# Kernel tuning notes

Hardware: AMD Instinct MI355X
Metric: run time of the kernel (lower is better)

## Reference

```python
import jax, jax.numpy as jnp
import numpy as np

STALK_DIM = 16
N_NODES = 50000
N_EDGES = 400000
HIDDEN = 64


def setup_inputs() -> dict:
    key = jax.random.key(0)
    k1, k2, k3, k4 = jax.random.split(key, 4)
    d = STALK_DIM
    x = jax.random.normal(k1, (N_NODES, d), dtype=jnp.float32)
    edge_index = jax.random.randint(k2, (2, N_EDGES), 0, N_NODES, dtype=jnp.int64)
    W1 = jax.random.normal(k3, (HIDDEN, 2 * d), dtype=jnp.float32) * (1.0 / np.sqrt(2 * d))
    b1 = jnp.zeros((HIDDEN,), dtype=jnp.float32)
    W2 = jax.random.normal(k4, (d, HIDDEN), dtype=jnp.float32) * (1.0 / np.sqrt(HIDDEN))
    b2 = jnp.zeros((d,), dtype=jnp.float32)
    return {"x": x, "edge_index": edge_index, "W1": W1, "b1": b1, "W2": W2, "b2": b2}


def reference(x, edge_index, W1, b1, W2, b2):
    d = x.shape[1]
    n = x.shape[0]
    src, dst = edge_index[0], edge_index[1]
    xs, xd = x[src], x[dst]  # [E, d]

    def reflection(a, b):
        h = jax.nn.relu(jnp.concatenate([a, b], axis=1) @ W1.T + b1)
        return h @ W2.T + b2  # [E, d]

    def householder(v):
        # F.normalize(v, dim=1): v / max(||v||, 1e-12)
        vn = v / jnp.maximum(jnp.linalg.norm(v, axis=1, keepdims=True), 1e-12)
        return jnp.eye(d, dtype=v.dtype)[None] - 2.0 * vn[:, :, None] * vn[:, None, :]

    F_s = householder(reflection(xs, xd))  # [E, d, d]
    F_d = householder(reflection(xd, xs))  # [E, d, d]
    L_sd = -jnp.einsum('eki,ekj->eij', F_s, F_d)  # -F_s^T @ F_d, [E, d, d]

    # degrees: both endpoints of every edge contribute 1
    ones_e = jnp.ones(src.shape[0], dtype=x.dtype)
    deg = jnp.zeros(n, dtype=x.dtype).at[src].add(ones_e).at[dst].add(ones_e)
    deg_inv_sqrt = 1.0 / jnp.sqrt(jnp.maximum(deg, 1e-5))
    # D_inv_sqrt is scalar*I per node, so normalization is a scalar coefficient per edge
    coef = deg_inv_sqrt[src] * deg_inv_sqrt[dst]  # [E]

    # out[s] -= D^-1/2_s L D^-1/2_d x[d] ; out[d] -= D^-1/2_d L^T D^-1/2_s x[s]
    msg_s = coef[:, None] * jnp.einsum('eij,ej->ei', L_sd, xd)  # goes to src
    msg_d = coef[:, None] * jnp.einsum('eji,ej->ei', L_sd, xs)  # goes to dst

    out = x - jnp.zeros_like(x).at[src].add(msg_s) - jnp.zeros_like(x).at[dst].add(msg_d)
    return jax.nn.relu(out)
```

## Files before the change

### kernel.cpp

```cpp
#include <hip/hip_runtime.h>
#include <hip/hip_bf16.h>
#include <hip/hip_fp16.h>

#define N_NODES 50000
#define N_EDGES 400000
#define D 16
#define HID 64

#define SCAN_B 256
#define SCAN_G ((N_NODES + SCAN_B - 1) / SCAN_B)

typedef unsigned short ushort_t;

#define CNT4_OFF  0
#define DEG_OFF   (4 * N_NODES)
#define OFF_OFF   (5 * N_NODES)
#define CUR_OFF   (6 * N_NODES + 1)
#define BS_OFF    (7 * N_NODES + 1)
#define MSG_OFF_I (((BS_OFF + SCAN_G) + 3) & ~3)
#define PREP_OFF  (MSG_OFF_I + 2 * N_EDGES * D)
#define PREP_DW   (64 * 64 + 16)
#define CSR_NEEDED_BYTES ((size_t)(PREP_OFF + PREP_DW) * 4 + 64)

#define FB_NDEG   (N_NODES)
#define FB_NACC   (N_NODES * D)
#define FB_FLAGS  (FB_NDEG + FB_NACC)

__device__ __forceinline__ float bf_bits(ushort_t us) {
    return __uint_as_float(((unsigned)us) << 16);
}
__device__ __forceinline__ float lo_bf(unsigned u) { return __uint_as_float(u << 16); }
__device__ __forceinline__ float hi_bf(unsigned u) { return __uint_as_float(u & 0xffff0000u); }
__device__ __forceinline__ ushort_t f2bf(float v) {
    unsigned u = __float_as_uint(v);
    unsigned r = (u + 0x7fffu + ((u >> 16) & 1u)) >> 16;
    return (ushort_t)r;
}
__device__ __forceinline__ float ld_f(const void* p, int idx, int f32) {
    return f32 ? ((const float*)p)[idx]
               : bf_bits(((const ushort_t*)p)[idx]);
}

__device__ __forceinline__ void load16(const void* __restrict__ p, long long base,
                                       int f32, float* o) {
    if (f32) {
        const float4* q = (const float4*)((const float*)p + base);
        float4 a = q[0], b = q[1], c = q[2], d = q[3];
        o[0]=a.x; o[1]=a.y; o[2]=a.z; o[3]=a.w;
        o[4]=b.x; o[5]=b.y; o[6]=b.z; o[7]=b.w;
        o[8]=c.x; o[9]=c.y; o[10]=c.z; o[11]=c.w;
        o[12]=d.x; o[13]=d.y; o[14]=d.z; o[15]=d.w;
    } else {
        const uint4* q = (const uint4*)((const ushort_t*)p + base);
        uint4 a = q[0], b = q[1];
        unsigned u[8] = {a.x, a.y, a.z, a.w, b.x, b.y, b.z, b.w};
#pragma unroll
        for (int k = 0; k < 8; k++) {
            o[2 * k]     = lo_bf(u[k]);
            o[2 * k + 1] = hi_bf(u[k]);
        }
    }
}

__device__ __forceinline__ void load_edge(const void* __restrict__ ei, int e, int is64,
                                          int& s, int& d) {
    if (is64) {
        const long long* p = (const long long*)ei;
        s = (int)p[e];
        d = (int)p[N_EDGES + e];
    } else {
        const int* p = (const int*)ei;
        s = p[e];
        d = p[N_EDGES + e];
    }
}

__device__ __forceinline__ void detect_flags_par(const void* x, const void* ei,
                                                 int* flags) {
    int t = threadIdx.x;
    if (t < 64) {
        const ushort_t* h = (const ushort_t*)x;
        int bad = 0;
#pragma unroll
        for (int k = 0; k < 4; k++) {
            float v = bf_bits(h[4 * t + k]);
            if (!(v == v) || fabsf(v) > 1.0e6f) bad = 1;
        }
        unsigned long long mb = __ballot(bad);
        const long long* p = (const long long*)ei;
        int bad64 = 0;
        if (t < 16) {
            long long v = p[t];
            bad64 = (v < 0 || v >= N_NODES) ? 1 : 0;
        }
        unsigned long long m64 = __ballot(bad64);
        if (t == 0) {
            flags[0] = mb ? 1 : 0;
            flags[1] = m64 ? 0 : 1;
        }
    }
}

__device__ __forceinline__ void stage_weights(
    const void* W1, const void* b1, const void* W2, const void* b2, int f32,
    float* sW1, float* sW2t, float* sb1, float* sb2)
{
    int t = threadIdx.x;
    for (int idx = t; idx < HID * 2 * D; idx += blockDim.x)
        sW1[idx] = ld_f(W1, idx, f32);
    for (int idx = t; idx < HID * D; idx += blockDim.x) {
        int j = idx / D, i = idx % D;
        sW2t[idx] = ld_f(W2, i * HID + j, f32);
    }
    if (t < HID) sb1[t] = ld_f(b1, t, f32);
    if (t < D)  sb2[t] = ld_f(b2, t, f32);
}

__device__ __forceinline__ void edge_math_v4(
    const float* __restrict__ sW1, const float* __restrict__ sW2t,
    const float* __restrict__ sb1, const float* __restrict__ sb2,
    const float* xs, const float* xd, float coef,
    float* ms, float* md)
{
    float vs[D], vd[D];
#pragma unroll
    for (int i = 0; i < D; i++) { vs[i] = sb2[i]; vd[i] = sb2[i]; }
#pragma unroll 4
    for (int j = 0; j < HID; j++) {
        float hs = sb1[j], hd = sb1[j];
        const float4* w4 = (const float4*)&sW1[j * 2 * D];
#pragma unroll
        for (int t = 0; t < 4; t++) {
            float4 wv = w4[t];
            int k = 4 * t;
            hs = fmaf(wv.x, xs[k],     hs); hd = fmaf(wv.x, xd[k],     hd);
            hs = fmaf(wv.y, xs[k + 1], hs); hd = fmaf(wv.y, xd[k + 1], hd);
            hs = fmaf(wv.z, xs[k + 2], hs); hd = fmaf(wv.z, xd[k + 2], hd);
            hs = fmaf(wv.w, xs[k + 3], hs); hd = fmaf(wv.w, xd[k + 3], hd);
        }
#pragma unroll
        for (int t = 0; t < 4; t++) {
            float4 wv = w4[4 + t];
            int k = 4 * t;
            hs = fmaf(wv.x, xd[k],     hs); hd = fmaf(wv.x, xs[k],     hd);
            hs = fmaf(wv.y, xd[k + 1], hs); hd = fmaf(wv.y, xs[k + 1], hd);
            hs = fmaf(wv.z, xd[k + 2], hs); hd = fmaf(wv.z, xs[k + 2], hd);
            hs = fmaf(wv.w, xd[k + 3], hs); hd = fmaf(wv.w, xs[k + 3], hd);
        }
        hs = fmaxf(hs, 0.0f);
        hd = fmaxf(hd, 0.0f);
        const float4* w24 = (const float4*)&sW2t[j * D];
#pragma unroll
        for (int t = 0; t < 4; t++) {
            float4 u = w24[t];
            int i = 4 * t;
            vs[i]     = fmaf(u.x, hs, vs[i]);     vd[i]     = fmaf(u.x, hd, vd[i]);
            vs[i + 1] = fmaf(u.y, hs, vs[i + 1]); vd[i + 1] = fmaf(u.y, hd, vd[i + 1]);
            vs[i + 2] = fmaf(u.z, hs, vs[i + 2]); vd[i + 2] = fmaf(u.z, hd, vd[i + 2]);
            vs[i + 3] = fmaf(u.w, hs, vs[i + 3]); vd[i + 3] = fmaf(u.w, hd, vd[i + 3]);
        }
    }
    float ns = 0.0f, nd = 0.0f;
#pragma unroll
    for (int i = 0; i < D; i++) { ns = fmaf(vs[i], vs[i], ns); nd = fmaf(vd[i], vd[i], nd); }
    float is_ = 1.0f / fmaxf(sqrtf(ns), 1e-12f);
    float id_ = 1.0f / fmaxf(sqrtf(nd), 1e-12f);
#pragma unroll
    for (int i = 0; i < D; i++) { vs[i] *= is_; vd[i] *= id_; }
    float dot1 = 0.0f;
#pragma unroll
    for (int i = 0; i < D; i++) dot1 = fmaf(vd[i], xd[i], dot1);
#pragma unroll
    for (int i = 0; i < D; i++) ms[i] = fmaf(-2.0f * dot1, vd[i], xd[i]);
    float dot2 = 0.0f;
#pragma unroll
    for (int i = 0; i < D; i++) dot2 = fmaf(vs[i], ms[i], dot2);
#pragma unroll
    for (int i = 0; i < D; i++) ms[i] = coef * fmaf(-2.0f * dot2, vs[i], ms[i]);
    float dot3 = 0.0f;
#pragma unroll
    for (int i = 0; i < D; i++) dot3 = fmaf(vs[i], xs[i], dot3);
#pragma unroll
    for (int i = 0; i < D; i++) md[i] = fmaf(-2.0f * dot3, vs[i], xs[i]);
    float dot4 = 0.0f;
#pragma unroll
    for (int i = 0; i < D; i++) dot4 = fmaf(vd[i], md[i], dot4);
#pragma unroll
    for (int i = 0; i < D; i++) md[i] = coef * fmaf(-2.0f * dot4, vd[i], md[i]);
}

__global__ void csr_count_kernel(const void* __restrict__ ei,
                                 const void* __restrict__ x,
                                 const void* __restrict__ W1,
                                 const void* __restrict__ b1,
                                 const void* __restrict__ W2,
                                 const void* __restrict__ b2,
                                 int* __restrict__ wsI) {
    __shared__ int sfl[2];
    detect_flags_par(x, ei, sfl);
    __syncthreads();
    int i64 = sfl[1];

    if (blockIdx.x == 0) {
        float* pf = (float*)(wsI + PREP_OFF);
        const ushort_t* W1b = (const ushort_t*)W1;
        const ushort_t* W2b = (const ushort_t*)W2;
        const ushort_t* b1b = (const ushort_t*)b1;
        const ushort_t* b2b = (const ushort_t*)b2;
        for (int idx = threadIdx.x; idx < 64 * 64; idx += 256) {
            int j = idx >> 6, w = idx & 63;
            float val = 0.0f;
            if (w < 32)      val = bf_bits(W1b[j * 32 + w]);
            else if (w < 48) val = bf_bits(W2b[(w - 32) * HID + j]);
            else if (w == 48) val = bf_bits(b1b[j]);
            pf[idx] = val;
        }
        if (threadIdx.x < D)
            pf[64 * 64 + threadIdx.x] = bf_bits(b2b[threadIdx.x]);
    }

    int e = blockIdx.x * blockDim.x + threadIdx.x;
    if (e >= N_EDGES) return;
    int s, d;
    load_edge(ei, e, i64, s, d);
    int r = (e & 3) * N_NODES;
    atomicAdd(&wsI[CNT4_OFF + r + s], 1);
    atomicAdd(&wsI[CNT4_OFF + r + d], 1);
}

__global__ __launch_bounds__(SCAN_B) void csr_scan1_kernel(int* __restrict__ wsI) {
    __shared__ int sm[SCAN_B];
    int t = threadIdx.x;
    int g = blockIdx.x * SCAN_B + t;
    int c = 0;
    if (g < N_NODES) {
        c = wsI[CNT4_OFF + g] + wsI[CNT4_OFF + N_NODES + g]
          + wsI[CNT4_OFF + 2 * N_NODES + g] + wsI[CNT4_OFF + 3 * N_NODES + g];
        wsI[DEG_OFF + g] = c;
    }
    sm[t] = c;
    __syncthreads();
    for (int st = SCAN_B / 2; st > 0; st >>= 1) {
        if (t < st) sm[t] += sm[t + st];
        __syncthreads();
    }
    if (t == 0) wsI[BS_OFF + blockIdx.x] = sm[0];
}

__global__ __launch_bounds__(SCAN_B) void csr_scan3_kernel(int* __restrict__ wsI) {
    __shared__ int sB[SCAN_B];
    __shared__ int sm[SCAN_B];
    int t = threadIdx.x;
    int bsv = (t < SCAN_G) ? wsI[BS_OFF + t] : 0;
    sB[t] = bsv;
    __syncthreads();
    for (int st = 1; st < SCAN_B; st <<= 1) {
        int u = (t >= st) ? sB[t - st] : 0;
        __syncthreads();
        sB[t] += u;
        __syncthreads();
    }
    int blockBase = sB[blockIdx.x] - wsI[BS_OFF + blockIdx.x];

    int g = blockIdx.x * SCAN_B + t;
    int c = (g < N_NODES) ? wsI[DEG_OFF + g] : 0;
    sm[t] = c;
    __syncthreads();
    for (int st = 1; st < SCAN_B; st <<= 1) {
        int u = (t >= st) ? sm[t - st] : 0;
        __syncthreads();
        sm[t] += u;
        __syncthreads();
    }
    int excl = sm[t] - c + blockBase;
    if (g < N_NODES) {
        wsI[OFF_OFF + g] = excl;
        wsI[CUR_OFF + g] = excl;
        if (g == N_NODES - 1) wsI[OFF_OFF + N_NODES] = excl + c;
    }
}

__global__ __launch_bounds__(256) void csr_edge_kernel(
    const void* __restrict__ x,
    const void* __restrict__ ei,
    const void* __restrict__ W1,
    const void* __restrict__ b1,
    const void* __restrict__ W2,
    const void* __restrict__ b2,
    const float* __restrict__ prep,
    int* __restrict__ wsI)
{
    __shared__ __align__(16) float sW1f[HID * 2 * D];
    __shared__ __align__(16) float sW2tf[HID * D];
    __shared__ float sb1[HID];
    __shared__ float sb2[D];
    __shared__ int sfl[2];

    detect_flags_par(x, ei, sfl);
    __syncthreads();
    int f32 = sfl[0], i64 = sfl[1];
    int t = threadIdx.x;

    if (f32) {
        for (int idx = t; idx < HID * 2 * D; idx += 256)
            sW1f[idx] = ld_f(W1, idx, 1);
        for (int idx = t; idx < HID * D; idx += 256) {
            int j = idx / D, i = idx % D;
            sW2tf[idx] = ld_f(W2, i * HID + j, 1);
        }
        if (t < HID) sb1[t] = ld_f(b1, t, 1);
        if (t < D)  sb2[t] = ld_f(b2, t, 1);
        __syncthreads();
    }

    int e = blockIdx.x * 256 + t;
    if (e >= N_EDGES) return;

    int s, d;
    load_edge(ei, e, i64, s, d);
    float degs = (float)wsI[DEG_OFF + s];
    float degd = (float)wsI[DEG_OFF + d];
    float coef = (1.0f / sqrtf(fmaxf(degs, 1e-5f))) * (1.0f / sqrtf(fmaxf(degd, 1e-5f)));
    float* msg = (float*)(wsI + MSG_OFF_I);

    float xs[D], xd[D];
    load16(x, (long long)s * D, f32, xs);
    load16(x, (long long)d * D, f32, xd);

    float ms[D], md[D];
    if (!f32) {
        const float* b2f = prep + 64 * 64;
        float vs[D], vd[D];
#pragma unroll
        for (int i = 0; i < D; i++) { vs[i] = b2f[i]; vd[i] = b2f[i]; }

#pragma unroll 1
        for (int j = 0; j < HID; j++) {
            const float* w = prep + (j << 6);
            float b1j = w[48];
            float hs0 = b1j, hs1 = 0.0f, hd0 = b1j, hd1 = 0.0f;
#pragma unroll
            for (int k = 0; k < 8; k++) {
                hs0 = fmaf(w[k],     xs[k],     hs0);
                hd0 = fmaf(w[k],     xd[k],     hd0);
                hs1 = fmaf(w[8 + k], xs[8 + k], hs1);
                hd1 = fmaf(w[8 + k], xd[8 + k], hd1);
            }
#pragma unroll
            for (int k = 0; k < 8; k++) {
                hs0 = fmaf(w[16 + k], xd[k],     hs0);
                hd0 = fmaf(w[16 + k], xs[k],     hd0);
                hs1 = fmaf(w[24 + k], xd[8 + k], hs1);
                hd1 = fmaf(w[24 + k], xs[8 + k], hd1);
            }
            float hs = fmaxf(hs0 + hs1, 0.0f);
            float hd = fmaxf(hd0 + hd1, 0.0f);
#pragma unroll
            for (int i = 0; i < D; i++) {
                vs[i] = fmaf(w[32 + i], hs, vs[i]);
                vd[i] = fmaf(w[32 + i], hd, vd[i]);
            }
        }

        float ns = 0.0f, nd = 0.0f;
#pragma unroll
        for (int i = 0; i < D; i++) { ns = fmaf(vs[i], vs[i], ns); nd = fmaf(vd[i], vd[i], nd); }
        float is_ = 1.0f / fmaxf(sqrtf(ns), 1e-12f);
        float id_ = 1.0f / fmaxf(sqrtf(nd), 1e-12f);
#pragma unroll
        for (int i = 0; i < D; i++) { vs[i] *= is_; vd[i] *= id_; }

        float dot1 = 0.0f;
#pragma unroll
        for (int i = 0; i < D; i++) dot1 = fmaf(vd[i], xd[i], dot1);
#pragma unroll
        for (int i = 0; i < D; i++) ms[i] = fmaf(-2.0f * dot1, vd[i], xd[i]);
        float dot2 = 0.0f;
#pragma unroll
        for (int i = 0; i < D; i++) dot2 = fmaf(vs[i], ms[i], dot2);
#pragma unroll
        for (int i = 0; i < D; i++) ms[i] = coef * fmaf(-2.0f * dot2, vs[i], ms[i]);
        float dot3 = 0.0f;
#pragma unroll
        for (int i = 0; i < D; i++) dot3 = fmaf(vs[i], xs[i], dot3);
#pragma unroll
        for (int i = 0; i < D; i++) md[i] = fmaf(-2.0f * dot3, vs[i], xs[i]);
        float dot4 = 0.0f;
#pragma unroll
        for (int i = 0; i < D; i++) dot4 = fmaf(vd[i], md[i], dot4);
#pragma unroll
        for (int i = 0; i < D; i++) md[i] = coef * fmaf(-2.0f * dot4, vd[i], md[i]);
    } else {
        edge_math_v4(sW1f, sW2tf, sb1, sb2, xs, xd, coef, ms, md);
    }

    int slot_s = atomicAdd(&wsI[CUR_OFF + s], 1);
    float4* m0 = (float4*)(msg + (long long)slot_s * D);
    m0[0] = make_float4(ms[0], ms[1], ms[2], ms[3]);
    m0[1] = make_float4(ms[4], ms[5], ms[6], ms[7]);
    m0[2] = make_float4(ms[8], ms[9], ms[10], ms[11]);
    m0[3] = make_float4(ms[12], ms[13], ms[14], ms[15]);
    int slot_d = atomicAdd(&wsI[CUR_OFF + d], 1);
    float4* m1 = (float4*)(msg + (long long)slot_d * D);
    m1[0] = make_float4(md[0], md[1], md[2], md[3]);
    m1[1] = make_float4(md[4], md[5], md[6], md[7]);
    m1[2] = make_float4(md[8], md[9], md[10], md[11]);
    m1[3] = make_float4(md[12], md[13], md[14], md[15]);
}

__global__ __launch_bounds__(256) void csr_gather_kernel(
    const void* __restrict__ x,
    const void* __restrict__ ei,
    const int* __restrict__ wsI,
    void* __restrict__ out)
{
    __shared__ int sfl[2];
    detect_flags_par(x, ei, sfl);
    __syncthreads();
    int f32 = sfl[0];

    int n = blockIdx.x * 64 + (threadIdx.x >> 2);
    int c = threadIdx.x & 3;
    if (n >= N_NODES) return;

    const int* off = wsI + OFF_OFF;
    const float4* msg4 = (const float4*)(wsI + MSG_OFF_I);

    int beg = off[n], end = off[n + 1];
    float4 a = make_float4(0.0f, 0.0f, 0.0f, 0.0f);
    int it = beg;
    for (; it + 2 <= end; it += 2) {
        float4 u = msg4[(long long)it * 4 + c];
        float4 v = msg4[(long long)(it + 1) * 4 + c];
        a.x += u.x + v.x; a.y += u.y + v.y; a.z += u.z + v.z; a.w += u.w + v.w;
    }
    if (it < end) {
        float4 u = msg4[(long long)it * 4 + c];
        a.x += u.x; a.y += u.y; a.z += u.z; a.w += u.w;
    }

    long long xb = (long long)n * D + 4 * c;
    float4 xv;
    if (f32) {
        xv = *(const float4*)((const float*)x + xb);
    } else {
        uint2 u = *(const uint2*)((const ushort_t*)x + xb);
        xv.x = lo_bf(u.x); xv.y = hi_bf(u.x);
        xv.z = lo_bf(u.y); xv.w = hi_bf(u.y);
    }
    float4 r;
    r.x = fmaxf(xv.x + a.x, 0.0f);
    r.y = fmaxf(xv.y + a.y, 0.0f);
    r.z = fmaxf(xv.z + a.z, 0.0f);
    r.w = fmaxf(xv.w + a.w, 0.0f);
    if (f32) {
        *(float4*)((float*)out + xb) = r;
    } else {
        uint2 o;
        o.x = (unsigned)f2bf(r.x) | ((unsigned)f2bf(r.y) << 16);
        o.y = (unsigned)f2bf(r.z) | ((unsigned)f2bf(r.w) << 16);
        *(uint2*)((ushort_t*)out + xb) = o;
    }
}

__global__ void fb_init_kernel(float* __restrict__ ws,
                               const void* __restrict__ x,
                               const void* __restrict__ ei) {
    int i = blockIdx.x * blockDim.x + threadIdx.x;
    if (i < FB_FLAGS) ws[i] = 0.0f;
    if (blockIdx.x == 0)
        detect_flags_par(x, ei, (int*)(ws + FB_FLAGS));
}

__global__ void fb_deg_kernel(const void* __restrict__ ei, float* __restrict__ ws) {
    int i64 = ((const int*)(ws + FB_FLAGS))[1];
    int e = blockIdx.x * blockDim.x + threadIdx.x;
    if (e >= N_EDGES) return;
    int s, d;
    load_edge(ei, e, i64, s, d);
    atomicAdd(&ws[s], 1.0f);
    atomicAdd(&ws[d], 1.0f);
}

__global__ __launch_bounds__(256) void fb_edge_kernel(
    const void* __restrict__ x, const void* __restrict__ ei,
    const void* __restrict__ W1, const void* __restrict__ b1,
    const void* __restrict__ W2, const void* __restrict__ b2,
    float* __restrict__ ws)
{
    __shared__ __align__(16) float sW1[HID * 2 * D];
    __shared__ __align__(16) float sW2t[HID * D];
    __shared__ float sb1[HID];
    __shared__ float sb2[D];
    const int* flags = (const int*)(ws + FB_FLAGS);
    int f32 = flags[0], i64 = flags[1];
    stage_weights(W1, b1, W2, b2, f32, sW1, sW2t, sb1, sb2);
    __syncthreads();
    int e = blockIdx.x * blockDim.x + threadIdx.x;
    if (e >= N_EDGES) return;
    int s, d;
    load_edge(ei, e, i64, s, d);
    float xs[D], xd[D];
    load16(x, (long long)s * D, f32, xs);
    load16(x, (long long)d * D, f32, xd);
    float coef = (1.0f / sqrtf(fmaxf(ws[s], 1e-5f))) * (1.0f / sqrtf(fmaxf(ws[d], 1e-5f)));
    float ms[D], md[D];
    edge_math_v4(sW1, sW2t, sb1, sb2, xs, xd, coef, ms, md);
    float* acc = ws + FB_NDEG;
#pragma unroll
    for (int i = 0; i < D; i++) atomicAdd(&acc[(long long)s * D + i], ms[i]);
#pragma unroll
    for (int i = 0; i < D; i++) atomicAdd(&acc[(long long)d * D + i], md[i]);
}

__global__ void fb_finalize_kernel(const void* __restrict__ x,
                                   const float* __restrict__ ws,
                                   void* __restrict__ out)
{
    int f32 = ((const int*)(ws + FB_FLAGS))[0];
    const float* acc = ws + FB_NDEG;
    int i = blockIdx.x * blockDim.x + threadIdx.x;
    if (i >= FB_NACC) return;
    float v = ld_f(x, i, f32) + acc[i];
    v = fmaxf(v, 0.0f);
    if (f32) ((float*)out)[i] = v;
    else     ((__hip_bfloat16*)out)[i] = __float2bfloat16(v);
}

extern "C" void kernel_launch(void* const* d_in, const int* in_sizes, int n_in,
                              void* d_out, int out_size, void* d_ws, size_t ws_size,
                              hipStream_t stream)
{
    const void* x  = d_in[0];
    const void* ei = d_in[1];
    const void* W1 = d_in[2];
    const void* b1 = d_in[3];
    const void* W2 = d_in[4];
    const void* b2 = d_in[5];

    int blk = 256;
    if (ws_size >= CSR_NEEDED_BYTES) {
        int* wsI = (int*)d_ws;
        hipMemsetAsync(d_ws, 0, (size_t)4 * N_NODES * sizeof(int), stream);
        csr_count_kernel<<<(N_EDGES + blk - 1) / blk, blk, 0, stream>>>(ei, x, W1, b1, W2, b2, wsI);
        csr_scan1_kernel<<<SCAN_G, SCAN_B, 0, stream>>>(wsI);
        csr_scan3_kernel<<<SCAN_G, SCAN_B, 0, stream>>>(wsI);
        csr_edge_kernel<<<(N_EDGES + blk - 1) / blk, blk, 0, stream>>>(
            x, ei, W1, b1, W2, b2, (const float*)(wsI + PREP_OFF), wsI);
        csr_gather_kernel<<<(N_NODES + 63) / 64, blk, 0, stream>>>(x, ei, wsI, d_out);
    } else {
        float* ws = (float*)d_ws;
        fb_init_kernel<<<(FB_FLAGS + blk - 1) / blk, blk, 0, stream>>>(ws, x, ei);
        fb_deg_kernel<<<(N_EDGES + blk - 1) / blk, blk, 0, stream>>>(ei, ws);
        fb_edge_kernel<<<(N_EDGES + blk - 1) / blk, blk, 0, stream>>>(x, ei, W1, b1, W2, b2, ws);
        fb_finalize_kernel<<<(FB_NACC + blk - 1) / blk, blk, 0, stream>>>(x, ws, d_out);
    }
}
```

Before: 204.7 us.

## Precompute per-node first-layer projections to avoid per-edge W1 matmul

Splits the first MLP layer W1·[a;b] into per-node halves A=W1a·x+b1 and B=W1b·x, computed once per node inside the scan kernel and stored in a new workspace region. The edge kernel then forms hidden units as relu(A[s]+B[d]) and relu(A[d]+B[s]), removing the 64x32 per-edge dot products and leaving only the second layer. In exchange each edge reads two 512-byte node rows, the workspace needs N*128 extra floats, and the path runs only for bf16 inputs when the workspace is large enough.

Result: no change. 205.8 us (+0.6%).

```diff
diff --git a/kernel.cpp b/kernel.cpp
--- a/kernel.cpp
+++ b/kernel.cpp
@@ -17,10 +17,13 @@
 #define OFF_OFF   (5 * N_NODES)
 #define CUR_OFF   (6 * N_NODES + 1)
 #define BS_OFF    (7 * N_NODES + 1)
-#define MSG_OFF_I (((BS_OFF + SCAN_G) + 3) & ~3)
+#define MSG_OFF_I (((BS_OFF + SCAN_G) + 15) & ~15)
 #define PREP_OFF  (MSG_OFF_I + 2 * N_EDGES * D)
-#define PREP_DW   (64 * 64 + 16)
-#define CSR_NEEDED_BYTES ((size_t)(PREP_OFF + PREP_DW) * 4 + 64)
+#define PREP_DW   (64 * 64 + 16 + 64 * 16)
+#define AB_OFF    (PREP_OFF + PREP_DW)
+#define AB_DW     (N_NODES * 2 * HID)
+#define CSR_NEEDED_BYTES ((size_t)(AB_OFF) * 4 + 64)
+#define NEW_NEEDED_BYTES ((size_t)(AB_OFF + AB_DW) * 4 + 64)
 
 #define FB_NDEG   (N_NODES)
 #define FB_NACC   (N_NODES * D)
@@ -189,211 +192,77 @@
     for (int i = 0; i < D; i++) md[i] = coef * fmaf(-2.0f * dot4, vd[i], md[i]);
 }
 
-__global__ void csr_count_kernel(const void* __restrict__ ei,
-                                 const void* __restrict__ x,
-                                 const void* __restrict__ W1,
-                                 const void* __restrict__ b1,
-                                 const void* __restrict__ W2,
-                                 const void* __restrict__ b2,
-                                 int* __restrict__ wsI) {
-    __shared__ int sfl[2];
-    detect_flags_par(x, ei, sfl);
-    __syncthreads();
-    int i64 = sfl[1];
-
-    if (blockIdx.x == 0) {
-        float* pf = (float*)(wsI + PREP_OFF);
-        const ushort_t* W1b = (const ushort_t*)W1;
-        const ushort_t* W2b = (const ushort_t*)W2;
-        const ushort_t* b1b = (const ushort_t*)b1;
-        const ushort_t* b2b = (const ushort_t*)b2;
-        for (int idx = threadIdx.x; idx < 64 * 64; idx += 256) {
-            int j = idx >> 6, w = idx & 63;
-            float val = 0.0f;
-            if (w < 32)      val = bf_bits(W1b[j * 32 + w]);
-            else if (w < 48) val = bf_bits(W2b[(w - 32) * HID + j]);
-            else if (w == 48) val = bf_bits(b1b[j]);
-            pf[idx] = val;
-        }
-        if (threadIdx.x < D)
-            pf[64 * 64 + threadIdx.x] = bf_bits(b2b[threadIdx.x]);
-    }
-
-    int e = blockIdx.x * blockDim.x + threadIdx.x;
-    if (e >= N_EDGES) return;
-    int s, d;
-    load_edge(ei, e, i64, s, d);
-    int r = (e & 3) * N_NODES;
-    atomicAdd(&wsI[CNT4_OFF + r + s], 1);
-    atomicAdd(&wsI[CNT4_OFF + r + d], 1);
-}
-
-__global__ __launch_bounds__(SCAN_B) void csr_scan1_kernel(int* __restrict__ wsI) {
-    __shared__ int sm[SCAN_B];
-    int t = threadIdx.x;
-    int g = blockIdx.x * SCAN_B + t;
-    int c = 0;
-    if (g < N_NODES) {
-        c = wsI[CNT4_OFF + g] + wsI[CNT4_OFF + N_NODES + g]
-          + wsI[CNT4_OFF + 2 * N_NODES + g] + wsI[CNT4_OFF + 3 * N_NODES + g];
-        wsI[DEG_OFF + g] = c;
-    }
-    sm[t] = c;
-    __syncthreads();
-    for (int st = SCAN_B / 2; st > 0; st >>= 1) {
-        if (t < st) sm[t] += sm[t + st];
-        __syncthreads();
-    }
-    if (t == 0) wsI[BS_OFF + blockIdx.x] = sm[0];
-}
-
-__global__ __launch_bounds__(SCAN_B) void csr_scan3_kernel(int* __restrict__ wsI) {
-    __shared__ int sB[SCAN_B];
-    __shared__ int sm[SCAN_B];
-    int t = threadIdx.x;
-    int bsv = (t < SCAN_G) ? wsI[BS_OFF + t] : 0;
-    sB[t] = bsv;
-    __syncthreads();
-    for (int st = 1; st < SCAN_B; st <<= 1) {
-        int u = (t >= st) ? sB[t - st] : 0;
-        __syncthreads();
-        sB[t] += u;
-        __syncthreads();
-    }
-    int blockBase = sB[blockIdx.x] - wsI[BS_OFF + blockIdx.x];
-
-    int g = blockIdx.x * SCAN_B + t;
-    int c = (g < N_NODES) ? wsI[DEG_OFF + g] : 0;
-    sm[t] = c;
-    __syncthreads();
-    for (int st = 1; st < SCAN_B; st <<= 1) {
-        int u = (t >= st) ? sm[t - st] : 0;
-        __syncthreads();
-        sm[t] += u;
-        __syncthreads();
-    }
-    int excl = sm[t] - c + blockBase;
-    if (g < N_NODES) {
-        wsI[OFF_OFF + g] = excl;
-        wsI[CUR_OFF + g] = excl;
-        if (g == N_NODES - 1) wsI[OFF_OFF + N_NODES] = excl + c;
-    }
-}
-
-__global__ __launch_bounds__(256) void csr_edge_kernel(
-    const void* __restrict__ x,
-    const void* __restrict__ ei,
-    const void* __restrict__ W1,
-    const void* __restrict__ b1,
-    const void* __restrict__ W2,
-    const void* __restrict__ b2,
+__device__ __forceinline__ void edge_math_prep(
     const float* __restrict__ prep,
-    int* __restrict__ wsI)
-{
-    __shared__ __align__(16) float sW1f[HID * 2 * D];
-    __shared__ __align__(16) float sW2tf[HID * D];
-    __shared__ float sb1[HID];
-    __shared__ float sb2[D];
-    __shared__ int sfl[2];
-
-    detect_flags_par(x, ei, sfl);
-    __syncthreads();
-    int f32 = sfl[0], i64 = sfl[1];
-    int t = threadIdx.x;
-
-    if (f32) {
-        for (int idx = t; idx < HID * 2 * D; idx += 256)
-            sW1f[idx] = ld_f(W1, idx, 1);
-        for (int idx = t; idx < HID * D; idx += 256) {
-            int j = idx / D, i = idx % D;
-            sW2tf[idx] = ld_f(W2, i * HID + j, 1);
-        }
-        if (t < HID) sb1[t] = ld_f(b1, t, 1);
-        if (t < D)  sb2[t] = ld_f(b2, t, 1);
-        __syncthreads();
-    }
-
-    int e = blockIdx.x * 256 + t;
-    if (e >= N_EDGES) return;
-
-    int s, d;
-    load_edge(ei, e, i64, s, d);
-    float degs = (float)wsI[DEG_OFF + s];
-    float degd = (float)wsI[DEG_OFF + d];
-    float coef = (1.0f / sqrtf(fmaxf(degs, 1e-5f))) * (1.0f / sqrtf(fmaxf(degd, 1e-5f)));
-    float* msg = (float*)(wsI + MSG_OFF_I);
-
-    float xs[D], xd[D];
-    load16(x, (long long)s * D, f32, xs);
-    load16(x, (long long)d * D, f32, xd);
-
-    float ms[D], md[D];
-    if (!f32) {
-        const float* b2f = prep + 64 * 64;
-        float vs[D], vd[D];
-#pragma unroll
-        for (int i = 0; i < D; i++) { vs[i] = b2f[i]; vd[i] = b2f[i]; }
+    const float* xs, const float* xd, float coef,
+    float* ms, float* md)
+{
+    const float* b2f = prep + 64 * 64;
+    float vs[D], vd[D];
+#pragma unroll
+    for (int i = 0; i < D; i++) { vs[i] = b2f[i]; vd[i] = b2f[i]; }
 
 #pragma unroll 1
-        for (int j = 0; j < HID; j++) {
-            const float* w = prep + (j << 6);
-            float b1j = w[48];
-            float hs0 = b1j, hs1 = 0.0f, hd0 = b1j, hd1 = 0.0f;
-#pragma unroll
-            for (int k = 0; k < 8; k++) {
-                hs0 = fmaf(w[k],     xs[k],     hs0);
-                hd0 = fmaf(w[k],     xd[k],     hd0);
-                hs1 = fmaf(w[8 + k], xs[8 + k], hs1);
-                hd1 = fmaf(w[8 + k], xd[8 + k], hd1);
-            }
-#pragma unroll
-            for (int k = 0; k < 8; k++) {
-                hs0 = fmaf(w[16 + k], xd[k],     hs0);
-                hd0 = fmaf(w[16 + k], xs[k],     hd0);
-                hs1 = fmaf(w[24 + k], xd[8 + k], hs1);
-                hd1 = fmaf(w[24 + k], xs[8 + k], hd1);
-            }
-            float hs = fmaxf(hs0 + hs1, 0.0f);
-            float hd = fmaxf(hd0 + hd1, 0.0f);
-#pragma unroll
-            for (int i = 0; i < D; i++) {
-                vs[i] = fmaf(w[32 + i], hs, vs[i]);
-                vd[i] = fmaf(w[32 + i], hd, vd[i]);
-            }
-        }
-
-        float ns = 0.0f, nd = 0.0f;
-#pragma unroll
-        for (int i = 0; i < D; i++) { ns = fmaf(vs[i], vs[i], ns); nd = fmaf(vd[i], vd[i], nd); }
-        float is_ = 1.0f / fmaxf(sqrtf(ns), 1e-12f);
-        float id_ = 1.0f / fmaxf(sqrtf(nd), 1e-12f);
-#pragma unroll
-        for (int i = 0; i < D; i++) { vs[i] *= is_; vd[i] *= id_; }
-
-        float dot1 = 0.0f;
-#pragma unroll
-        for (int i = 0; i < D; i++) dot1 = fmaf(vd[i], xd[i], dot1);
-#pragma unroll
-        for (int i = 0; i < D; i++) ms[i] = fmaf(-2.0f * dot1, vd[i], xd[i]);
-        float dot2 = 0.0f;
-#pragma unroll
-        for (int i = 0; i < D; i++) dot2 = fmaf(vs[i], ms[i], dot2);
-#pragma unroll
-        for (int i = 0; i < D; i++) ms[i] = coef * fmaf(-2.0f * dot2, vs[i], ms[i]);
-        float dot3 = 0.0f;
-#pragma unroll
-        for (int i = 0; i < D; i++) dot3 = fmaf(vs[i], xs[i], dot3);
-#pragma unroll
-        for (int i = 0; i < D; i++) md[i] = fmaf(-2.0f * dot3, vs[i], xs[i]);
-        float dot4 = 0.0f;
-#pragma unroll
-        for (int i = 0; i < D; i++) dot4 = fmaf(vd[i], md[i], dot4);
-#pragma unroll
-        for (int i = 0; i < D; i++) md[i] = coef * fmaf(-2.0f * dot4, vd[i], md[i]);
-    } else {
-        edge_math_v4(sW1f, sW2tf, sb1, sb2, xs, xd, coef, ms, md);
-    }
-
+    for (int j = 0; j < HID; j++) {
+        const float* w = prep + (j << 6);
+        float b1j = w[48];
+        float hs0 = b1j, hs1 = 0.0f, hd0 = b1j, hd1 = 0.0f;
+#pragma unroll
+        for (int k = 0; k < 8; k++) {
+            hs0 = fmaf(w[k],     xs[k],     hs0);
+            hd0 = fmaf(w[k],     xd[k],     hd0);
+            hs1 = fmaf(w[8 + k], xs[8 + k], hs1);
+            hd1 = fmaf(w[8 + k], xd[8 + k], hd1);
+        }
+#pragma unroll
+        for (int k = 0; k < 8; k++) {
+            hs0 = fmaf(w[16 + k], xd[k],     hs0);
+            hd0 = fmaf(w[16 + k], xs[k],     hd0);
+            hs1 = fmaf(w[24 + k], xd[8 + k], hs1);
+            hd1 = fmaf(w[24 + k], xs[8 + k], hd1);
+        }
+        float hs = fmaxf(hs0 + hs1, 0.0f);
+        float hd = fmaxf(hd0 + hd1, 0.0f);
+#pragma unroll
+        for (int i = 0; i < D; i++) {
+            vs[i] = fmaf(w[32 + i], hs, vs[i]);
+            vd[i] = fmaf(w[32 + i], hd, vd[i]);
+        }
+    }
+
+    float ns = 0.0f, nd = 0.0f;
+#pragma unroll
+    for (int i = 0; i < D; i++) { ns = fmaf(vs[i], vs[i], ns); nd = fmaf(vd[i], vd[i], nd); }
+    float is_ = 1.0f / fmaxf(sqrtf(ns), 1e-12f);
+    float id_ = 1.0f / fmaxf(sqrtf(nd), 1e-12f);
+#pragma unroll
+    for (int i = 0; i < D; i++) { vs[i] *= is_; vd[i] *= id_; }
+
+    float dot1 = 0.0f;
+#pragma unroll
+    for (int i = 0; i < D; i++) dot1 = fmaf(vd[i], xd[i], dot1);
+#pragma unroll
+    for (int i = 0; i < D; i++) ms[i] = fmaf(-2.0f * dot1, vd[i], xd[i]);
+    float dot2 = 0.0f;
+#pragma unroll
+    for (int i = 0; i < D; i++) dot2 = fmaf(vs[i], ms[i], dot2);
+#pragma unroll
+    for (int i = 0; i < D; i++) ms[i] = coef * fmaf(-2.0f * dot2, vs[i], ms[i]);
+    float dot3 = 0.0f;
+#pragma unroll
+    for (int i = 0; i < D; i++) dot3 = fmaf(vs[i], xs[i], dot3);
+#pragma unroll
+    for (int i = 0; i < D; i++) md[i] = fmaf(-2.0f * dot3, vs[i], xs[i]);
+    float dot4 = 0.0f;
+#pragma unroll
+    for (int i = 0; i < D; i++) dot4 = fmaf(vd[i], md[i], dot4);
+#pragma unroll
+    for (int i = 0; i < D; i++) md[i] = coef * fmaf(-2.0f * dot4, vd[i], md[i]);
+}
+
+__device__ __forceinline__ void write_msgs(int* __restrict__ wsI, float* __restrict__ msg,
+                                           int s, int d, const float* ms, const float* md)
+{
     int slot_s = atomicAdd(&wsI[CUR_OFF + s], 1);
     float4* m0 = (float4*)(msg + (long long)slot_s * D);
     m0[0] = make_float4(ms[0], ms[1], ms[2], ms[3]);
@@ -408,21 +277,36 @@
     m1[3] = make_float4(md[12], md[13], md[14], md[15]);
 }
 
-__global__ __launch_bounds__(256) void csr_gather_kernel(
-    const void* __restrict__ x,
-    const void* __restrict__ ei,
-    const int* __restrict__ wsI,
-    void* __restrict__ out)
-{
-    __shared__ int sfl[2];
-    detect_flags_par(x, ei, sfl);
-    __syncthreads();
-    int f32 = sfl[0];
-
-    int n = blockIdx.x * 64 + (threadIdx.x >> 2);
-    int c = threadIdx.x & 3;
-    if (n >= N_NODES) return;
-
+__device__ __forceinline__ void pack_prep(const void* W1, const void* b1,
+                                          const void* W2, const void* b2,
+                                          int* __restrict__ wsI)
+{
+    float* pf = (float*)(wsI + PREP_OFF);
+    const ushort_t* W1b = (const ushort_t*)W1;
+    const ushort_t* W2b = (const ushort_t*)W2;
+    const ushort_t* b1b = (const ushort_t*)b1;
+    const ushort_t* b2b = (const ushort_t*)b2;
+    for (int idx = threadIdx.x; idx < 64 * 64; idx += 256) {
+        int j = idx >> 6, w = idx & 63;
+        float val = 0.0f;
+        if (w < 32)      val = bf_bits(W1b[j * 32 + w]);
+        else if (w < 48) val = bf_bits(W2b[(w - 32) * HID + j]);
+        else if (w == 48) val = bf_bits(b1b[j]);
+        pf[idx] = val;
+    }
+    if (threadIdx.x < D)
+        pf[64 * 64 + threadIdx.x] = bf_bits(b2b[threadIdx.x]);
+    for (int idx = threadIdx.x; idx < HID * D; idx += 256) {
+        int j = idx >> 4, i = idx & 15;
+        pf[64 * 64 + 16 + idx] = bf_bits(W2b[i * HID + j]);
+    }
+}
+
+__device__ __forceinline__ void gather_node(int n, int c, int f32,
+                                            const int* __restrict__ wsI,
+                                            const void* __restrict__ x,
+                                            void* __restrict__ out)
+{
     const int* off = wsI + OFF_OFF;
     const float4* msg4 = (const float4*)(wsI + MSG_OFF_I);
 
@@ -463,6 +347,258 @@
     }
 }
 
+__global__ void csr_count_kernel(const void* __restrict__ ei,
+                                 const void* __restrict__ x,
+                                 const void* __restrict__ W1,
+                                 const void* __restrict__ b1,
+                                 const void* __restrict__ W2,
+                                 const void* __restrict__ b2,
+                                 int* __restrict__ wsI) {
+    __shared__ int sfl[2];
+    detect_flags_par(x, ei, sfl);
+    __syncthreads();
+    int i64 = sfl[1];
+
+    if (blockIdx.x == 0) pack_prep(W1, b1, W2, b2, wsI);
+
+    int e = blockIdx.x * blockDim.x + threadIdx.x;
+    if (e >= N_EDGES) return;
+    int s, d;
+    load_edge(ei, e, i64, s, d);
+    int r = (e & 3) * N_NODES;
+    atomicAdd(&wsI[CNT4_OFF + r + s], 1);
+    atomicAdd(&wsI[CNT4_OFF + r + d], 1);
+}
+
+__global__ __launch_bounds__(SCAN_B) void csr_scan1_kernel(
+    int* __restrict__ wsI,
+    const void* __restrict__ x,
+    const void* __restrict__ ei,
+    const void* __restrict__ W1,
+    const void* __restrict__ b1,
+    int useAB)
+{
+    __shared__ int sm[SCAN_B];
+    __shared__ int sfl[2];
+    detect_flags_par(x, ei, sfl);
+    __syncthreads();
+    int f32 = sfl[0];
+
+    int t = threadIdx.x;
+    int g = blockIdx.x * SCAN_B + t;
+    int c = 0;
+    if (g < N_NODES) {
+        c = wsI[CNT4_OFF + g] + wsI[CNT4_OFF + N_NODES + g]
+          + wsI[CNT4_OFF + 2 * N_NODES + g] + wsI[CNT4_OFF + 3 * N_NODES + g];
+        wsI[DEG_OFF + g] = c;
+    }
+    sm[t] = c;
+    __syncthreads();
+    for (int st = SCAN_B / 2; st > 0; st >>= 1) {
+        if (t < st) sm[t] += sm[t + st];
+        __syncthreads();
+    }
+    if (t == 0) wsI[BS_OFF + blockIdx.x] = sm[0];
+
+    if (useAB && !f32 && g < N_NODES) {
+        const ushort_t* b1b = (const ushort_t*)b1;
+        const unsigned* W1w = (const unsigned*)W1;
+        float xr[D];
+        load16(x, (long long)g * D, 0, xr);
+        float* ab = (float*)(wsI + AB_OFF) + (long long)g * 2 * HID;
+#pragma unroll 1
+        for (int j4 = 0; j4 < 16; j4++) {
+            float4 a4, b4;
+#pragma unroll
+            for (int r = 0; r < 4; r++) {
+                int j = 4 * j4 + r;
+                const unsigned* w = W1w + j * 16;
+                float a = bf_bits(b1b[j]);
+                float bb = 0.0f;
+#pragma unroll
+                for (int k = 0; k < 8; k++) {
+                    unsigned wk = w[k];
+                    a = fmaf(lo_bf(wk), xr[2 * k],     a);
+                    a = fmaf(hi_bf(wk), xr[2 * k + 1], a);
+                }
+#pragma unroll
+                for (int k = 0; k < 8; k++) {
+                    unsigned wk = w[8 + k];
+                    bb = fmaf(lo_bf(wk), xr[2 * k],     bb);
+                    bb = fmaf(hi_bf(wk), xr[2 * k + 1], bb);
+                }
+                (&a4.x)[r] = a;
+                (&b4.x)[r] = bb;
+            }
+            *(float4*)(ab + 4 * j4)       = a4;
+            *(float4*)(ab + HID + 4 * j4) = b4;
+        }
+    }
+}
+
+__global__ __launch_bounds__(SCAN_B) void csr_scan3_kernel(int* __restrict__ wsI) {
+    __shared__ int sB[SCAN_B];
+    __shared__ int sm[SCAN_B];
+    int t = threadIdx.x;
+    int bsv = (t < SCAN_G) ? wsI[BS_OFF + t] : 0;
+    sB[t] = bsv;
+    __syncthreads();
+    for (int st = 1; st < SCAN_B; st <<= 1) {
+        int u = (t >= st) ? sB[t - st] : 0;
+        __syncthreads();
+        sB[t] += u;
+        __syncthreads();
+    }
+    int blockBase = sB[blockIdx.x] - wsI[BS_OFF + blockIdx.x];
+
+    int g = blockIdx.x * SCAN_B + t;
+    int c = (g < N_NODES) ? wsI[DEG_OFF + g] : 0;
+    sm[t] = c;
+    __syncthreads();
+    for (int st = 1; st < SCAN_B; st <<= 1) {
+        int u = (t >= st) ? sm[t - st] : 0;
+        __syncthreads();
+        sm[t] += u;
+        __syncthreads();
+    }
+    int excl = sm[t] - c + blockBase;
+    if (g < N_NODES) {
+        wsI[OFF_OFF + g] = excl;
+        wsI[CUR_OFF + g] = excl;
+        if (g == N_NODES - 1) wsI[OFF_OFF + N_NODES] = excl + c;
+    }
+}
+
+__global__ __launch_bounds__(256) void csr_edge_kernel(
+    const void* __restrict__ x,
+    const void* __restrict__ ei,
+    const void* __restrict__ W1,
+    const void* __restrict__ b1,
+    const void* __restrict__ W2,
+    const void* __restrict__ b2,
+    const float* __restrict__ prep,
+    int* __restrict__ wsI,
+    int useAB)
+{
+    __shared__ __align__(16) float sW1f[HID * 2 * D];
+    __shared__ __align__(16) float sW2tf[HID * D];
+    __shared__ float sb1[HID];
+    __shared__ float sb2[D];
+    __shared__ int sfl[2];
+
+    detect_flags_par(x, ei, sfl);
+    __syncthreads();
+    int f32 = sfl[0], i64 = sfl[1];
+    int t = threadIdx.x;
+
+    if (f32) {
+        stage_weights(W1, b1, W2, b2, 1, sW1f, sW2tf, sb1, sb2);
+        __syncthreads();
+    }
+
+    int e = blockIdx.x * 256 + t;
+    if (e >= N_EDGES) return;
+
+    int s, d;
+    load_edge(ei, e, i64, s, d);
+    float degs = (float)wsI[DEG_OFF + s];
+    float degd = (float)wsI[DEG_OFF + d];
+    float coef = (1.0f / sqrtf(fmaxf(degs, 1e-5f))) * (1.0f / sqrtf(fmaxf(degd, 1e-5f)));
+    float* msg = (float*)(wsI + MSG_OFF_I);
+
+    if (!f32 && useAB) {
+        const float* AB = (const float*)(wsI + AB_OFF);
+        const float* ns_ = AB + (long long)s * 2 * HID;
+        const float* nd_ = AB + (long long)d * 2 * HID;
+        const float* b2f = prep + 64 * 64;
+        const float* w2t = prep + 64 * 64 + 16;
+
+        float vs[D], vd[D];
+#pragma unroll
+        for (int i = 0; i < D; i++) { vs[i] = b2f[i]; vd[i] = b2f[i]; }
+
+#pragma unroll 1
+        for (int jj = 0; jj < 16; jj++) {
+            float4 as4 = *(const float4*)(ns_ + 4 * jj);
+            float4 bs4 = *(const float4*)(ns_ + HID + 4 * jj);
+            float4 ad4 = *(const float4*)(nd_ + 4 * jj);
+            float4 bd4 = *(const float4*)(nd_ + HID + 4 * jj);
+#pragma unroll
+            for (int r = 0; r < 4; r++) {
+                const float* w2 = w2t + (4 * jj + r) * D;
+                float hs = fmaxf((&as4.x)[r] + (&bd4.x)[r], 0.0f);
+                float hd = fmaxf((&ad4.x)[r] + (&bs4.x)[r], 0.0f);
+#pragma unroll
+                for (int i = 0; i < D; i++) {
+                    vs[i] = fmaf(w2[i], hs, vs[i]);
+                    vd[i] = fmaf(w2[i], hd, vd[i]);
+                }
+            }
+        }
+
+        float xs[D], xd[D];
+        load16(x, (long long)s * D, 0, xs);
+        load16(x, (long long)d * D, 0, xd);
+
+        float ns = 0.0f, nd = 0.0f;
+#pragma unroll
+        for (int i = 0; i < D; i++) { ns = fmaf(vs[i], vs[i], ns); nd = fmaf(vd[i], vd[i], nd); }
+        float is_ = 1.0f / fmaxf(sqrtf(ns), 1e-12f);
+        float id_ = 1.0f / fmaxf(sqrtf(nd), 1e-12f);
+#pragma unroll
+        for (int i = 0; i < D; i++) { vs[i] *= is_; vd[i] *= id_; }
+
+        float ms[D], md[D];
+        float dot1 = 0.0f;
+#pragma unroll
+        for (int i = 0; i < D; i++) dot1 = fmaf(vd[i], xd[i], dot1);
+#pragma unroll
+        for (int i = 0; i < D; i++) ms[i] = fmaf(-2.0f * dot1, vd[i], xd[i]);
+        float dot2 = 0.0f;
+#pragma unroll
+        for (int i = 0; i < D; i++) dot2 = fmaf(vs[i], ms[i], dot2);
+#pragma unroll
+        for (int i = 0; i < D; i++) ms[i] = coef * fmaf(-2.0f * dot2, vs[i], ms[i]);
+        float dot3 = 0.0f;
+#pragma unroll
+        for (int i = 0; i < D; i++) dot3 = fmaf(vs[i], xs[i], dot3);
+#pragma unroll
+        for (int i = 0; i < D; i++) md[i] = fmaf(-2.0f * dot3, vs[i], xs[i]);
+        float dot4 = 0.0f;
+#pragma unroll
+        for (int i = 0; i < D; i++) dot4 = fmaf(vd[i], md[i], dot4);
+#pragma unroll
+        for (int i = 0; i < D; i++) md[i] = coef * fmaf(-2.0f * dot4, vd[i], md[i]);
+
+        write_msgs(wsI, msg, s, d, ms, md);
+    } else {
+        float xs[D], xd[D];
+        load16(x, (long long)s * D, f32, xs);
+        load16(x, (long long)d * D, f32, xd);
+        float ms[D], md[D];
+        if (!f32) edge_math_prep(prep, xs, xd, coef, ms, md);
+        else      edge_math_v4(sW1f, sW2tf, sb1, sb2, xs, xd, coef, ms, md);
+        write_msgs(wsI, msg, s, d, ms, md);
+    }
+}
+
+__global__ __launch_bounds__(256) void csr_gather_kernel(
+    const void* __restrict__ x,
+    const void* __restrict__ ei,
+    const int* __restrict__ wsI,
+    void* __restrict__ out)
+{
+    __shared__ int sfl[2];
+    detect_flags_par(x, ei, sfl);
+    __syncthreads();
+    int f32 = sfl[0];
+
+    int n = blockIdx.x * 64 + (threadIdx.x >> 2);
+    int c = threadIdx.x & 3;
+    if (n >= N_NODES) return;
+    gather_node(n, c, f32, wsI, x, out);
+}
+
 __global__ void fb_init_kernel(float* __restrict__ ws,
                                const void* __restrict__ x,
                                const void* __restrict__ ei) {
@@ -540,13 +676,15 @@
 
     int blk = 256;
     if (ws_size >= CSR_NEEDED_BYTES) {
+        int useAB = (ws_size >= NEW_NEEDED_BYTES) ? 1 : 0;
         int* wsI = (int*)d_ws;
         hipMemsetAsync(d_ws, 0, (size_t)4 * N_NODES * sizeof(int), stream);
-        csr_count_kernel<<<(N_EDGES + blk - 1) / blk, blk, 0, stream>>>(ei, x, W1, b1, W2, b2, wsI);
-        csr_scan1_kernel<<<SCAN_G, SCAN_B, 0, stream>>>(wsI);
+        csr_count_kernel<<<(N_EDGES + blk - 1) / blk, blk, 0, stream>>>(
+            ei, x, W1, b1, W2, b2, wsI);
+        csr_scan1_kernel<<<SCAN_G, SCAN_B, 0, stream>>>(wsI, x, ei, W1, b1, useAB);
         csr_scan3_kernel<<<SCAN_G, SCAN_B, 0, stream>>>(wsI);
         csr_edge_kernel<<<(N_EDGES + blk - 1) / blk, blk, 0, stream>>>(
-            x, ei, W1, b1, W2, b2, (const float*)(wsI + PREP_OFF), wsI);
+            x, ei, W1, b1, W2, b2, (const float*)(wsI + PREP_OFF), wsI, useAB);
         csr_gather_kernel<<<(N_NODES + 63) / 64, blk, 0, stream>>>(x, ei, wsI, d_out);
     } else {
         float* ws = (float*)d_ws;
```
